# Optimization experiments

Measured on AMD Instinct MI355X. Metric: run time of the kernel, lower is better.

The kernel has to match this reference:

```python
import jax, jax.numpy as jnp
import numpy as np

N_NODES = 100000
N_EDGES = 1600000
IN_DIM = 128
HID_DIM = 128
OUT_DIM = 64


def _glorot(key, shape):
    fan_in, fan_out = shape
    lim = float(np.sqrt(6.0 / (fan_in + fan_out)))
    return jax.random.uniform(key, shape, jnp.float32, -lim, lim)


def setup_inputs() -> dict:
    key = jax.random.key(0)
    ks = jax.random.split(key, 8)
    x = jax.random.normal(ks[0], (N_NODES, IN_DIM), jnp.float32)
    edge_index = jax.random.randint(ks[1], (2, N_EDGES), 0, N_NODES, jnp.int64)
    edge_weight = jax.random.uniform(ks[2], (N_EDGES,), jnp.float32)
    W1 = _glorot(ks[3], (IN_DIM, HID_DIM))
    b1 = jnp.zeros((HID_DIM,), jnp.float32)
    W2 = _glorot(ks[4], (HID_DIM, HID_DIM))
    b2 = jnp.zeros((HID_DIM,), jnp.float32)
    W3 = _glorot(ks[5], (HID_DIM, OUT_DIM))
    b3 = jnp.zeros((OUT_DIM,), jnp.float32)
    return {"x": x, "edge_index": edge_index, "edge_weight": edge_weight,
            "W1": W1, "b1": b1, "W2": W2, "b2": b2, "W3": W3, "b3": b3}


def gcn_conv(x, src, dst, ew, W, b, n_nodes):
    # torch_geometric GCNConv: add self-loops (weight 1), symmetric normalization,
    # linear transform (no bias) then aggregate, then add bias.
    xw = x @ W                                            # [N, out]
    deg = jax.ops.segment_sum(ew, dst, num_segments=n_nodes) + 1.0  # self-loop
    dis = jax.lax.rsqrt(deg)                              # deg >= 1, safe
    norm = dis[src] * ew * dis[dst]                       # [E]
    agg = jax.ops.segment_sum(norm[:, None] * xw[src], dst, num_segments=n_nodes)
    # self-loop contribution: norm_ii = dis_i^2 * 1.0
    return agg + (dis * dis)[:, None] * xw + b


def reference(x, edge_index, edge_weight, W1, b1, W2, b2, W3, b3):
    src, dst = edge_index[0], edge_index[1]
    n = x.shape[0]
    h = gcn_conv(x, src, dst, edge_weight, W1, b1, n)
    h = jax.nn.relu(h)  # dropout is identity at inference
    h = gcn_conv(h, src, dst, edge_weight, W2, b2, n)
    h = jax.nn.relu(h)
    out = gcn_conv(h, src, dst, edge_weight, W3, b3, n)
    return out
```

## Files before the change

### kernel.cpp

```cpp
#include <hip/hip_runtime.h>


typedef __attribute__((ext_vector_type(8))) short bf16x8;
typedef __attribute__((ext_vector_type(4))) float f32x4;

__device__ inline unsigned short f2bf(float f) {
  unsigned int u = __float_as_uint(f);
  u += 0x7fffu + ((u >> 16) & 1u);
  return (unsigned short)(u >> 16);
}

__global__ void init_kernel(const int* __restrict__ ei, int* __restrict__ flag,
                            int* __restrict__ pz, int n) {
  if (blockIdx.x == 0) {
    __shared__ int nonzero;
    if (threadIdx.x == 0) nonzero = 0;
    __syncthreads();
    int acc = 0;
#pragma unroll
    for (int it = 0; it < 8; ++it) {
      const int j = threadIdx.x + (it << 8);
      acc |= ei[2 * j + 1];
    }
    if (acc != 0) atomicOr(&nonzero, 1);
    __syncthreads();
    if (threadIdx.x == 0) flag[0] = (nonzero == 0) ? 1 : 0;
  }
  int i = blockIdx.x * blockDim.x + threadIdx.x;
  const int stride = gridDim.x * blockDim.x;
  for (; i < n; i += stride) pz[i] = 0;
}

__global__ void count_deg_pack(const int* __restrict__ ei, const int* __restrict__ flag,
                               const float* __restrict__ ew,
                               unsigned long long* __restrict__ packed,
                               int* __restrict__ eseq, int E) {
  const int e = blockIdx.x * blockDim.x + threadIdx.x;
  if (e >= E) return;
  const int use64 = flag[0];
  const int d = use64 ? ei[2 * (E + e)] : ei[E + e];
  const unsigned int fx = (unsigned int)(ew[e] * 16777216.0f);
  const unsigned long long old =
      atomicAdd(&packed[d], (1ULL << 32) | (unsigned long long)fx);
  eseq[e] = (int)(old >> 32);
}

__global__ __launch_bounds__(256)
void scan_phase1(const unsigned long long* __restrict__ packed,
                 int* __restrict__ bsums, int N) {
  __shared__ int red[256];
  const int t = threadIdx.x;
  const int base = blockIdx.x * 1024 + t * 4;
  int s = 0;
#pragma unroll
  for (int j = 0; j < 4; ++j) {
    const int idx = base + j;
    if (idx < N) s += (int)(packed[idx] >> 32);
  }
  red[t] = s;
  __syncthreads();
  for (int off = 128; off > 0; off >>= 1) {
    if (t < off) red[t] += red[t + off];
    __syncthreads();
  }
  if (t == 0) bsums[blockIdx.x] = red[0];
}

__global__ __launch_bounds__(1024)
void scan_phase2(int* __restrict__ bsums, int* __restrict__ row_start, int B, int N) {
  __shared__ int s[1024];
  const int t = threadIdx.x;
  const int v = (t < B) ? bsums[t] : 0;
  s[t] = v;
  __syncthreads();
  for (int off = 1; off < 1024; off <<= 1) {
    const int add = (t >= off) ? s[t - off] : 0;
    __syncthreads();
    s[t] += add;
    __syncthreads();
  }
  if (t < B) bsums[t] = s[t] - v;
  if (t == B - 1) row_start[N] = s[t];
}

__global__ __launch_bounds__(256)
void scan_phase3_dis(const unsigned long long* __restrict__ packed,
                     const int* __restrict__ bsums, int* __restrict__ row_start,
                     float* __restrict__ dis, int N) {
  __shared__ int tsum[256];
  const int t = threadIdx.x;
  const int base = blockIdx.x * 1024 + t * 4;
  unsigned long long pk[4];
  int v[4];
#pragma unroll
  for (int j = 0; j < 4; ++j) {
    pk[j] = (base + j < N) ? packed[base + j] : 0ULL;
    v[j] = (int)(pk[j] >> 32);
  }
  const int tot = v[0] + v[1] + v[2] + v[3];
  tsum[t] = tot;
  __syncthreads();
  for (int off = 1; off < 256; off <<= 1) {
    const int add = (t >= off) ? tsum[t - off] : 0;
    __syncthreads();
    tsum[t] += add;
    __syncthreads();
  }
  int run = bsums[blockIdx.x] + tsum[t] - tot;
#pragma unroll
  for (int j = 0; j < 4; ++j) {
    const int idx = base + j;
    if (idx < N) {
      row_start[idx] = run;
      run += v[j];
      const float deg = (float)(unsigned int)pk[j] * (1.0f / 16777216.0f);
      dis[idx] = rsqrtf(deg + 1.0f);
    }
  }
}

__global__ void fill_csr(const int* __restrict__ ei, const int* __restrict__ flag,
                         const float* __restrict__ ew, const float* __restrict__ dis,
                         const int* __restrict__ row_start, const int* __restrict__ eseq,
                         int2* __restrict__ csr, int E) {
  const int e = blockIdx.x * blockDim.x + threadIdx.x;
  if (e >= E) return;
  const int use64 = flag[0];
  const int s = use64 ? ei[2 * e] : ei[e];
  const int d = use64 ? ei[2 * (E + e)] : ei[E + e];
  const float nm = dis[s] * ew[e] * dis[d];
  const int pos = row_start[d] + eseq[e];
  csr[pos] = make_int2(s, __float_as_int(nm));
}

__global__ __launch_bounds__(256)
void prep_bf16(const float* __restrict__ W1, const float* __restrict__ W2,
               const float* __restrict__ W3, unsigned short* __restrict__ Wt1,
               unsigned short* __restrict__ Wt2, unsigned short* __restrict__ Wt3,
               const float* __restrict__ x, unsigned short* __restrict__ xbf,
               long long n4) {
  const int WTB = 160;
  if (blockIdx.x < WTB) {
    const int idx = blockIdx.x * 256 + threadIdx.x;
    if (idx < 16384) {
      const int m = idx >> 7, k = idx & 127;
      Wt1[idx] = f2bf(W1[k * 128 + m]);
    } else if (idx < 32768) {
      const int l = idx - 16384;
      const int m = l >> 7, k = l & 127;
      Wt2[l] = f2bf(W2[k * 128 + m]);
    } else {
      const int l = idx - 32768;
      const int m = l >> 7, k = l & 127;
      Wt3[l] = f2bf(W3[k * 64 + m]);
    }
    return;
  }
  long long i = (long long)(blockIdx.x - WTB) * 256 + threadIdx.x;
  const long long stride = (long long)(gridDim.x - WTB) * 256;
  for (; i < n4; i += stride) {
    const float4 v = ((const float4*)x)[i];
    ushort4 o;
    o.x = f2bf(v.x); o.y = f2bf(v.y); o.z = f2bf(v.z); o.w = f2bf(v.w);
    ((ushort4*)xbf)[i] = o;
  }
}

template <int M>
__global__ __launch_bounds__(256)
void gemm_mfma(const unsigned short* __restrict__ A, const unsigned short* __restrict__ Bt,
               unsigned short* __restrict__ C, int N) {
  const int lane = threadIdx.x & 63;
  const int m = lane & 15;
  const int q = lane >> 4;
  const int row0 = (blockIdx.x << 6) + ((threadIdx.x >> 6) << 4);

  const bool rowok = (row0 + m) < N;
  const unsigned short* arow = A + (long long)(row0 + m) * 128 + q * 8;
  bf16x8 a[4];
  const bf16x8 zf = {0, 0, 0, 0, 0, 0, 0, 0};
#pragma unroll
  for (int kt = 0; kt < 4; ++kt)
    a[kt] = rowok ? *(const bf16x8*)(arow + kt * 32) : zf;

#pragma unroll
  for (int ct = 0; ct < M / 16; ++ct) {
    f32x4 acc = {0.f, 0.f, 0.f, 0.f};
    const unsigned short* brow = Bt + (ct * 16 + m) * 128 + q * 8;
#pragma unroll
    for (int kt = 0; kt < 4; ++kt) {
      const bf16x8 b = *(const bf16x8*)(brow + kt * 32);
      acc = __builtin_amdgcn_mfma_f32_16x16x32_bf16(a[kt], b, acc, 0, 0, 0);
    }
#pragma unroll
    for (int r = 0; r < 4; ++r) {
      const int row = row0 + q * 4 + r;
      if (row < N) C[(long long)row * M + ct * 16 + m] = f2bf(acc[r]);
    }
  }
}

template <int M, bool RELU, bool OUTBF>
__global__ __launch_bounds__(256)
void gather(const int2* __restrict__ csr, const int* __restrict__ row_start,
            const unsigned short* __restrict__ xw, const float* __restrict__ dis,
            const float* __restrict__ bias, void* __restrict__ outp, int N) {
  const int node = (blockIdx.x << 2) + (threadIdx.x >> 6);
  const int lane = threadIdx.x & 63;
  if (node >= N) return;
  const int beg = __builtin_amdgcn_readfirstlane(row_start[node]);
  const int end = __builtin_amdgcn_readfirstlane(row_start[node + 1]);
  if (M == 128) {
    const int c = lane << 1;
    float2 a0 = make_float2(0.f, 0.f), a1 = a0, a2 = a0, a3 = a0;
    int e = beg;
    for (; e + 7 < end; e += 8) {
      int2 p[8];
      unsigned int u[8];
#pragma unroll
      for (int j = 0; j < 8; ++j) p[j] = csr[e + j];
#pragma unroll
      for (int j = 0; j < 8; ++j)
        u[j] = *(const unsigned int*)(xw + (long long)p[j].x * 128 + c);
#pragma unroll
      for (int j = 0; j < 8; ++j) {
        const float nm = __int_as_float(p[j].y);
        float2& ac = (j & 4) ? ((j & 2) ? a3 : a2) : ((j & 2) ? a1 : a0);
        ac.x = fmaf(nm, __uint_as_float(u[j] << 16), ac.x);
        ac.y = fmaf(nm, __uint_as_float(u[j] & 0xffff0000u), ac.y);
      }
    }
    for (; e + 1 < end; e += 2) {
      const int2 p0 = csr[e], p1 = csr[e + 1];
      const unsigned int u0 = *(const unsigned int*)(xw + (long long)p0.x * 128 + c);
      const unsigned int u1 = *(const unsigned int*)(xw + (long long)p1.x * 128 + c);
      const float n0 = __int_as_float(p0.y), n1 = __int_as_float(p1.y);
      a0.x = fmaf(n0, __uint_as_float(u0 << 16), a0.x);
      a0.y = fmaf(n0, __uint_as_float(u0 & 0xffff0000u), a0.y);
      a1.x = fmaf(n1, __uint_as_float(u1 << 16), a1.x);
      a1.y = fmaf(n1, __uint_as_float(u1 & 0xffff0000u), a1.y);
    }
    if (e < end) {
      const int2 p = csr[e];
      const float nm = __int_as_float(p.y);
      const unsigned int u = *(const unsigned int*)(xw + (long long)p.x * 128 + c);
      a2.x = fmaf(nm, __uint_as_float(u << 16), a2.x);
      a2.y = fmaf(nm, __uint_as_float(u & 0xffff0000u), a2.y);
    }
    float2 acc;
    acc.x = (a0.x + a1.x) + (a2.x + a3.x);
    acc.y = (a0.y + a1.y) + (a2.y + a3.y);
    const float di = dis[node];
    const float dsq = di * di;
    const unsigned int su = *(const unsigned int*)(xw + (long long)node * 128 + c);
    const float2 bv = *(const float2*)(bias + c);
    acc.x = fmaf(dsq, __uint_as_float(su << 16), acc.x) + bv.x;
    acc.y = fmaf(dsq, __uint_as_float(su & 0xffff0000u), acc.y) + bv.y;
    if (RELU) { acc.x = fmaxf(acc.x, 0.f); acc.y = fmaxf(acc.y, 0.f); }
    if (OUTBF) {
      const unsigned int pk =
          (unsigned int)f2bf(acc.x) | ((unsigned int)f2bf(acc.y) << 16);
      ((unsigned int*)outp)[(long long)node * 64 + lane] = pk;
    } else {
      *(float2*)((float*)outp + (long long)node * 128 + c) = acc;
    }
  } else {
    float a0 = 0.f, a1 = 0.f, a2 = 0.f, a3 = 0.f;
    int e = beg;
    for (; e + 7 < end; e += 8) {
      int2 p[8];
      unsigned int v[8];
#pragma unroll
      for (int j = 0; j < 8; ++j) p[j] = csr[e + j];
#pragma unroll
      for (int j = 0; j < 8; ++j) v[j] = xw[(long long)p[j].x * 64 + lane];
#pragma unroll
      for (int j = 0; j < 8; ++j) {
        float& ac = (j & 4) ? ((j & 2) ? a3 : a2) : ((j & 2) ? a1 : a0);
        ac = fmaf(__int_as_float(p[j].y), __uint_as_float(v[j] << 16), ac);
      }
    }
    for (; e < end; ++e) {
      const int2 p = csr[e];
      const unsigned int v = xw[(long long)p.x * 64 + lane];
      a0 = fmaf(__int_as_float(p.y), __uint_as_float(v << 16), a0);
    }
    float acc = (a0 + a1) + (a2 + a3);
    const float di = dis[node];
    const unsigned int sv = xw[(long long)node * 64 + lane];
    float r = fmaf(di * di, __uint_as_float(sv << 16), acc) + bias[lane];
    if (RELU) r = fmaxf(r, 0.f);
    ((float*)outp)[(long long)node * 64 + lane] = r;
  }
}

extern "C" void kernel_launch(void* const* d_in, const int* in_sizes, int n_in,
                              void* d_out, int out_size, void* d_ws, size_t ws_size,
                              hipStream_t stream) {
  const float* x  = (const float*)d_in[0];
  const int*   ei = (const int*)d_in[1];
  const float* ew = (const float*)d_in[2];
  const float* W1 = (const float*)d_in[3];
  const float* b1 = (const float*)d_in[4];
  const float* W2 = (const float*)d_in[5];
  const float* b2 = (const float*)d_in[6];
  const float* W3 = (const float*)d_in[7];
  const float* b3 = (const float*)d_in[8];
  float* out = (float*)d_out;

  const int IN = 128;
  const int N = in_sizes[0] / IN;
  const int E = in_sizes[2];

  char* ws = (char*)d_ws;
  unsigned long long* packed = (unsigned long long*)(ws);
  float* dis       = (float*)(ws + (1u << 20));
  int*   flag      = (int*)(ws + (1536u << 10));
  int*   bsums     = (int*)(ws + (1536u << 10) + 4096);
  int*   row_start = (int*)(ws + (1600u << 10));
  int2*  csr       = (int2*)(ws + (2560u << 10));
  unsigned short* Wt1 = (unsigned short*)(ws + (15872u << 10));
  unsigned short* Wt2 = (unsigned short*)(ws + (15872u << 10) + (128u << 10));
  unsigned short* Wt3 = (unsigned short*)(ws + (15872u << 10) + (256u << 10));
  unsigned short* bufA = (unsigned short*)(ws + (16u << 20));
  unsigned short* hbf  = (unsigned short*)(ws + (42u << 20));
  int* eseq = (int*)bufA;

  const dim3 blk(256);
  const int gE = (E + 255) / 256;
  const int B = (N + 1023) / 1024;

  hipLaunchKernelGGL(init_kernel, dim3(128), blk, 0, stream, ei, flag, (int*)packed, 2 * N);
  hipLaunchKernelGGL(count_deg_pack, dim3(gE), blk, 0, stream, ei, flag, ew, packed, eseq, E);
  hipLaunchKernelGGL(scan_phase1, dim3(B), blk, 0, stream, packed, bsums, N);
  hipLaunchKernelGGL(scan_phase2, dim3(1), dim3(1024), 0, stream, bsums, row_start, B, N);
  hipLaunchKernelGGL(scan_phase3_dis, dim3(B), blk, 0, stream, packed, bsums, row_start, dis, N);
  hipLaunchKernelGGL(fill_csr, dim3(gE), blk, 0, stream, ei, flag, ew, dis, row_start, eseq, csr, E);
  hipLaunchKernelGGL(prep_bf16, dim3(160 + 2048), blk, 0, stream,
                     W1, W2, W3, Wt1, Wt2, Wt3, x, hbf, (long long)N * 32);

  const int gGemm = (N + 63) / 64;
  const int gGather = (N + 3) / 4;

  hipLaunchKernelGGL((gemm_mfma<128>), dim3(gGemm), blk, 0, stream, hbf, Wt1, bufA, N);
  hipLaunchKernelGGL((gather<128, true, true>), dim3(gGather), blk, 0, stream,
                     csr, row_start, bufA, dis, b1, hbf, N);
  hipLaunchKernelGGL((gemm_mfma<128>), dim3(gGemm), blk, 0, stream, hbf, Wt2, bufA, N);
  hipLaunchKernelGGL((gather<128, true, true>), dim3(gGather), blk, 0, stream,
                     csr, row_start, bufA, dis, b2, hbf, N);
  hipLaunchKernelGGL((gemm_mfma<64>), dim3(gGemm), blk, 0, stream, hbf, Wt3, bufA, N);
  hipLaunchKernelGGL((gather<64, false, false>), dim3(gGather), blk, 0, stream,
                     csr, row_start, bufA, dis, b3, out, N);
}
```

Measured before the change: 495.5 us.

## Privatize degree-count atomics into 16 copies to reduce atomic contention

The packed degree/count atomics are spread over 16 per-block-group copies of the per-node counter array, so fewer threads contend on the same address. The scan phases then sum across the copies, and a per-copy offset table (coff) gives each edge its CSR slot. This adds a 16x larger array to zero and scan, plus extra memory traffic for the coff writes and reads. With about 16 edges per node spread over 100k nodes, contention may already be low, so the extra traffic can outweigh the benefit.

```diff
diff --git a/kernel.cpp b/kernel.cpp
--- a/kernel.cpp
+++ b/kernel.cpp
@@ -3,6 +3,8 @@
 
 typedef __attribute__((ext_vector_type(8))) short bf16x8;
 typedef __attribute__((ext_vector_type(4))) float f32x4;
+
+#define NCOPY 16
 
 __device__ inline unsigned short f2bf(float f) {
   unsigned int u = __float_as_uint(f);
@@ -33,29 +35,33 @@
 
 __global__ void count_deg_pack(const int* __restrict__ ei, const int* __restrict__ flag,
                                const float* __restrict__ ew,
-                               unsigned long long* __restrict__ packed,
-                               int* __restrict__ eseq, int E) {
+                               unsigned long long* __restrict__ packedC,
+                               int* __restrict__ eseq, int E, int N) {
   const int e = blockIdx.x * blockDim.x + threadIdx.x;
   if (e >= E) return;
   const int use64 = flag[0];
   const int d = use64 ? ei[2 * (E + e)] : ei[E + e];
   const unsigned int fx = (unsigned int)(ew[e] * 16777216.0f);
+  const size_t slot = (size_t)(blockIdx.x & (NCOPY - 1)) * N + d;
   const unsigned long long old =
-      atomicAdd(&packed[d], (1ULL << 32) | (unsigned long long)fx);
+      atomicAdd(&packedC[slot], (1ULL << 32) | (unsigned long long)fx);
   eseq[e] = (int)(old >> 32);
 }
 
 __global__ __launch_bounds__(256)
-void scan_phase1(const unsigned long long* __restrict__ packed,
+void scan_phase1(const unsigned long long* __restrict__ packedC,
                  int* __restrict__ bsums, int N) {
   __shared__ int red[256];
   const int t = threadIdx.x;
   const int base = blockIdx.x * 1024 + t * 4;
   int s = 0;
 #pragma unroll
-  for (int j = 0; j < 4; ++j) {
-    const int idx = base + j;
-    if (idx < N) s += (int)(packed[idx] >> 32);
+  for (int c = 0; c < NCOPY; ++c) {
+#pragma unroll
+    for (int j = 0; j < 4; ++j) {
+      const int idx = base + j;
+      if (idx < N) s += (int)(packedC[(size_t)c * N + idx] >> 32);
+    }
   }
   red[t] = s;
   __syncthreads();
@@ -84,18 +90,32 @@
 }
 
 __global__ __launch_bounds__(256)
-void scan_phase3_dis(const unsigned long long* __restrict__ packed,
+void scan_phase3_dis(const unsigned long long* __restrict__ packedC,
                      const int* __restrict__ bsums, int* __restrict__ row_start,
-                     float* __restrict__ dis, int N) {
+                     int* __restrict__ coff, float* __restrict__ dis, int N) {
   __shared__ int tsum[256];
   const int t = threadIdx.x;
   const int base = blockIdx.x * 1024 + t * 4;
-  unsigned long long pk[4];
+  int cnt[NCOPY][4];
+  unsigned long long deglo[4] = {0ULL, 0ULL, 0ULL, 0ULL};
+#pragma unroll
+  for (int c = 0; c < NCOPY; ++c) {
+#pragma unroll
+    for (int j = 0; j < 4; ++j) {
+      const int idx = base + j;
+      const unsigned long long p =
+          (idx < N) ? packedC[(size_t)c * N + idx] : 0ULL;
+      cnt[c][j] = (int)(p >> 32);
+      deglo[j] += (unsigned long long)(unsigned int)p;
+    }
+  }
   int v[4];
 #pragma unroll
   for (int j = 0; j < 4; ++j) {
-    pk[j] = (base + j < N) ? packed[base + j] : 0ULL;
-    v[j] = (int)(pk[j] >> 32);
+    int s = 0;
+#pragma unroll
+    for (int c = 0; c < NCOPY; ++c) s += cnt[c][j];
+    v[j] = s;
   }
   const int tot = v[0] + v[1] + v[2] + v[3];
   tsum[t] = tot;
@@ -112,8 +132,14 @@
     const int idx = base + j;
     if (idx < N) {
       row_start[idx] = run;
+      int b = run;
+#pragma unroll
+      for (int c = 0; c < NCOPY; ++c) {
+        coff[(size_t)c * N + idx] = b;
+        b += cnt[c][j];
+      }
       run += v[j];
-      const float deg = (float)(unsigned int)pk[j] * (1.0f / 16777216.0f);
+      const float deg = (float)deglo[j] * (1.0f / 16777216.0f);
       dis[idx] = rsqrtf(deg + 1.0f);
     }
   }
@@ -121,15 +147,15 @@
 
 __global__ void fill_csr(const int* __restrict__ ei, const int* __restrict__ flag,
                          const float* __restrict__ ew, const float* __restrict__ dis,
-                         const int* __restrict__ row_start, const int* __restrict__ eseq,
-                         int2* __restrict__ csr, int E) {
+                         const int* __restrict__ coff, const int* __restrict__ eseq,
+                         int2* __restrict__ csr, int E, int N) {
   const int e = blockIdx.x * blockDim.x + threadIdx.x;
   if (e >= E) return;
   const int use64 = flag[0];
   const int s = use64 ? ei[2 * e] : ei[e];
   const int d = use64 ? ei[2 * (E + e)] : ei[E + e];
   const float nm = dis[s] * ew[e] * dis[d];
-  const int pos = row_start[d] + eseq[e];
+  const int pos = coff[(size_t)(blockIdx.x & (NCOPY - 1)) * N + d] + eseq[e];
   csr[pos] = make_int2(s, __float_as_int(nm));
 }
 
@@ -313,7 +339,6 @@
   const int E = in_sizes[2];
 
   char* ws = (char*)d_ws;
-  unsigned long long* packed = (unsigned long long*)(ws);
   float* dis       = (float*)(ws + (1u << 20));
   int*   flag      = (int*)(ws + (1536u << 10));
   int*   bsums     = (int*)(ws + (1536u << 10) + 4096);
@@ -324,18 +349,24 @@
   unsigned short* Wt3 = (unsigned short*)(ws + (15872u << 10) + (256u << 10));
   unsigned short* bufA = (unsigned short*)(ws + (16u << 20));
   unsigned short* hbf  = (unsigned short*)(ws + (42u << 20));
+  unsigned long long* packedC = (unsigned long long*)(ws + (68u << 20));
+  int* coff = (int*)(ws + (81u << 20));
   int* eseq = (int*)bufA;
 
   const dim3 blk(256);
   const int gE = (E + 255) / 256;
   const int B = (N + 1023) / 1024;
 
-  hipLaunchKernelGGL(init_kernel, dim3(128), blk, 0, stream, ei, flag, (int*)packed, 2 * N);
-  hipLaunchKernelGGL(count_deg_pack, dim3(gE), blk, 0, stream, ei, flag, ew, packed, eseq, E);
-  hipLaunchKernelGGL(scan_phase1, dim3(B), blk, 0, stream, packed, bsums, N);
+  hipLaunchKernelGGL(init_kernel, dim3(2048), blk, 0, stream, ei, flag,
+                     (int*)packedC, NCOPY * 2 * N);
+  hipLaunchKernelGGL(count_deg_pack, dim3(gE), blk, 0, stream, ei, flag, ew,
+                     packedC, eseq, E, N);
+  hipLaunchKernelGGL(scan_phase1, dim3(B), blk, 0, stream, packedC, bsums, N);
   hipLaunchKernelGGL(scan_phase2, dim3(1), dim3(1024), 0, stream, bsums, row_start, B, N);
-  hipLaunchKernelGGL(scan_phase3_dis, dim3(B), blk, 0, stream, packed, bsums, row_start, dis, N);
-  hipLaunchKernelGGL(fill_csr, dim3(gE), blk, 0, stream, ei, flag, ew, dis, row_start, eseq, csr, E);
+  hipLaunchKernelGGL(scan_phase3_dis, dim3(B), blk, 0, stream, packedC, bsums,
+                     row_start, coff, dis, N);
+  hipLaunchKernelGGL(fill_csr, dim3(gE), blk, 0, stream, ei, flag, ew, dis,
+                     coff, eseq, csr, E, N);
   hipLaunchKernelGGL(prep_bf16, dim3(160 + 2048), blk, 0, stream,
                      W1, W2, W3, Wt1, Wt2, Wt3, x, hbf, (long long)N * 32);
 
```

Measured after the change: 518.8 us. +4.7%, slower.

## Build CSR via two-level binning instead of global per-node atomics

Applied to the files above, without the earlier changes.

Replaces per-edge 64-bit global atomics on per-node degree counters with a bucketed counting sort. Edges are first histogrammed into 128-node bins per chunk in shared memory, scanned, and scattered to binned order. A per-bin kernel then computes degrees, row starts and dis with shared-memory atomics and writes the CSR, and a final pass folds in dis[src]. This targets contended global atomics and random scatter in graph preprocessing, at the cost of more kernels and an extra pass over the edges.

```diff
diff --git a/kernel.cpp b/kernel.cpp
--- a/kernel.cpp
+++ b/kernel.cpp
@@ -3,6 +3,8 @@
 
 typedef __attribute__((ext_vector_type(8))) short bf16x8;
 typedef __attribute__((ext_vector_type(4))) float f32x4;
+
+#define CHUNK 4096
 
 __device__ inline unsigned short f2bf(float f) {
   unsigned int u = __float_as_uint(f);
@@ -10,53 +12,48 @@
   return (unsigned short)(u >> 16);
 }
 
-__global__ void init_kernel(const int* __restrict__ ei, int* __restrict__ flag,
-                            int* __restrict__ pz, int n) {
-  if (blockIdx.x == 0) {
-    __shared__ int nonzero;
-    if (threadIdx.x == 0) nonzero = 0;
-    __syncthreads();
-    int acc = 0;
-#pragma unroll
-    for (int it = 0; it < 8; ++it) {
-      const int j = threadIdx.x + (it << 8);
-      acc |= ei[2 * j + 1];
-    }
-    if (acc != 0) atomicOr(&nonzero, 1);
-    __syncthreads();
-    if (threadIdx.x == 0) flag[0] = (nonzero == 0) ? 1 : 0;
-  }
-  int i = blockIdx.x * blockDim.x + threadIdx.x;
-  const int stride = gridDim.x * blockDim.x;
-  for (; i < n; i += stride) pz[i] = 0;
-}
-
-__global__ void count_deg_pack(const int* __restrict__ ei, const int* __restrict__ flag,
-                               const float* __restrict__ ew,
-                               unsigned long long* __restrict__ packed,
-                               int* __restrict__ eseq, int E) {
-  const int e = blockIdx.x * blockDim.x + threadIdx.x;
-  if (e >= E) return;
+__global__ void init_flag(const int* __restrict__ ei, int* __restrict__ flag) {
+  __shared__ int nonzero;
+  if (threadIdx.x == 0) nonzero = 0;
+  __syncthreads();
+  int acc = 0;
+#pragma unroll
+  for (int it = 0; it < 8; ++it) acc |= ei[2 * (threadIdx.x + (it << 8)) + 1];
+  if (acc != 0) atomicOr(&nonzero, 1);
+  __syncthreads();
+  if (threadIdx.x == 0) flag[0] = (nonzero == 0) ? 1 : 0;
+}
+
+__global__ __launch_bounds__(256)
+void bin_hist(const int* __restrict__ ei, const int* __restrict__ flag,
+              int* __restrict__ mat, int E, int NB, int NBLK) {
+  __shared__ int hist[1024];
+  const int t = threadIdx.x;
+  for (int i = t; i < NB; i += 256) hist[i] = 0;
+  __syncthreads();
   const int use64 = flag[0];
-  const int d = use64 ? ei[2 * (E + e)] : ei[E + e];
-  const unsigned int fx = (unsigned int)(ew[e] * 16777216.0f);
-  const unsigned long long old =
-      atomicAdd(&packed[d], (1ULL << 32) | (unsigned long long)fx);
-  eseq[e] = (int)(old >> 32);
-}
-
-__global__ __launch_bounds__(256)
-void scan_phase1(const unsigned long long* __restrict__ packed,
-                 int* __restrict__ bsums, int N) {
+  const int base = blockIdx.x * CHUNK;
+#pragma unroll
+  for (int it = 0; it < CHUNK / 256; ++it) {
+    const int e = base + t + it * 256;
+    if (e < E) {
+      const int d = use64 ? ei[2 * (E + e)] : ei[E + e];
+      atomicAdd(&hist[d >> 7], 1);
+    }
+  }
+  __syncthreads();
+  for (int i = t; i < NB; i += 256) mat[i * NBLK + blockIdx.x] = hist[i];
+}
+
+__global__ __launch_bounds__(256)
+void scan_phase1(const int* __restrict__ mat, int* __restrict__ bsums, int L) {
   __shared__ int red[256];
   const int t = threadIdx.x;
   const int base = blockIdx.x * 1024 + t * 4;
   int s = 0;
 #pragma unroll
-  for (int j = 0; j < 4; ++j) {
-    const int idx = base + j;
-    if (idx < N) s += (int)(packed[idx] >> 32);
-  }
+  for (int j = 0; j < 4; ++j)
+    if (base + j < L) s += mat[base + j];
   red[t] = s;
   __syncthreads();
   for (int off = 128; off > 0; off >>= 1) {
@@ -84,19 +81,13 @@
 }
 
 __global__ __launch_bounds__(256)
-void scan_phase3_dis(const unsigned long long* __restrict__ packed,
-                     const int* __restrict__ bsums, int* __restrict__ row_start,
-                     float* __restrict__ dis, int N) {
+void scan_phase3(int* __restrict__ mat, const int* __restrict__ bsums, int L) {
   __shared__ int tsum[256];
   const int t = threadIdx.x;
   const int base = blockIdx.x * 1024 + t * 4;
-  unsigned long long pk[4];
   int v[4];
 #pragma unroll
-  for (int j = 0; j < 4; ++j) {
-    pk[j] = (base + j < N) ? packed[base + j] : 0ULL;
-    v[j] = (int)(pk[j] >> 32);
-  }
+  for (int j = 0; j < 4; ++j) v[j] = (base + j < L) ? mat[base + j] : 0;
   const int tot = v[0] + v[1] + v[2] + v[3];
   tsum[t] = tot;
   __syncthreads();
@@ -109,28 +100,98 @@
   int run = bsums[blockIdx.x] + tsum[t] - tot;
 #pragma unroll
   for (int j = 0; j < 4; ++j) {
-    const int idx = base + j;
-    if (idx < N) {
-      row_start[idx] = run;
-      run += v[j];
-      const float deg = (float)(unsigned int)pk[j] * (1.0f / 16777216.0f);
-      dis[idx] = rsqrtf(deg + 1.0f);
-    }
-  }
-}
-
-__global__ void fill_csr(const int* __restrict__ ei, const int* __restrict__ flag,
-                         const float* __restrict__ ew, const float* __restrict__ dis,
-                         const int* __restrict__ row_start, const int* __restrict__ eseq,
-                         int2* __restrict__ csr, int E) {
+    if (base + j < L) { mat[base + j] = run; run += v[j]; }
+  }
+}
+
+__global__ __launch_bounds__(256)
+void bin_scatter(const int* __restrict__ ei, const int* __restrict__ flag,
+                 const float* __restrict__ ew, const int* __restrict__ mat,
+                 int2* __restrict__ binned, int E, int NB, int NBLK) {
+  __shared__ int boff[1024];
+  __shared__ int cur[1024];
+  const int t = threadIdx.x;
+  for (int i = t; i < NB; i += 256) {
+    boff[i] = mat[i * NBLK + blockIdx.x];
+    cur[i] = 0;
+  }
+  __syncthreads();
+  const int use64 = flag[0];
+  const int base = blockIdx.x * CHUNK;
+#pragma unroll
+  for (int it = 0; it < CHUNK / 256; ++it) {
+    const int e = base + t + it * 256;
+    if (e < E) {
+      const int s = use64 ? ei[2 * e] : ei[e];
+      const int d = use64 ? ei[2 * (E + e)] : ei[E + e];
+      const int b = d >> 7;
+      const int r = atomicAdd(&cur[b], 1);
+      binned[boff[b] + r] = make_int2(s | ((d & 127) << 17), __float_as_int(ew[e]));
+    }
+  }
+}
+
+__global__ __launch_bounds__(256)
+void bucket_finalize(const int2* __restrict__ binned, const int* __restrict__ mat,
+                     int* __restrict__ row_start, float* __restrict__ dis,
+                     int2* __restrict__ csr, int E, int N, int NB, int NBLK) {
+  __shared__ int cnt[128];
+  __shared__ unsigned int fxs[128];
+  __shared__ int sc[128];
+  __shared__ int rowb[128];
+  __shared__ float disl[128];
+  __shared__ int cur[128];
+  const int t = threadIdx.x;
+  const int b = blockIdx.x;
+  const int beg = mat[b * NBLK];
+  const int end = (b == NB - 1) ? E : mat[(b + 1) * NBLK];
+  if (t < 128) { cnt[t] = 0; fxs[t] = 0u; }
+  __syncthreads();
+  for (int i = beg + t; i < end; i += 256) {
+    const int2 r = binned[i];
+    const int dl = (r.x >> 17) & 127;
+    atomicAdd(&cnt[dl], 1);
+    atomicAdd(&fxs[dl], (unsigned int)(__int_as_float(r.y) * 16777216.0f));
+  }
+  __syncthreads();
+  if (t < 128) sc[t] = cnt[t];
+  __syncthreads();
+  for (int off = 1; off < 128; off <<= 1) {
+    const int v = (t < 128 && t >= off) ? sc[t - off] : 0;
+    __syncthreads();
+    if (t < 128) sc[t] += v;
+    __syncthreads();
+  }
+  if (t < 128) {
+    const int node = (b << 7) + t;
+    const int rb = beg + sc[t] - cnt[t];
+    rowb[t] = rb;
+    cur[t] = 0;
+    if (node < N) {
+      row_start[node] = rb;
+      const float deg = (float)fxs[t] * (1.0f / 16777216.0f);
+      const float di = rsqrtf(deg + 1.0f);
+      dis[node] = di;
+      disl[t] = di;
+    }
+  }
+  __syncthreads();
+  for (int i = beg + t; i < end; i += 256) {
+    const int2 r = binned[i];
+    const int dl = (r.x >> 17) & 127;
+    const int rk = atomicAdd(&cur[dl], 1);
+    csr[rowb[dl] + rk] =
+        make_int2(r.x & 0x1FFFF, __float_as_int(__int_as_float(r.y) * disl[dl]));
+  }
+}
+
+__global__ __launch_bounds__(256)
+void norm_fold(int2* __restrict__ csr, const float* __restrict__ dis, int E) {
   const int e = blockIdx.x * blockDim.x + threadIdx.x;
   if (e >= E) return;
-  const int use64 = flag[0];
-  const int s = use64 ? ei[2 * e] : ei[e];
-  const int d = use64 ? ei[2 * (E + e)] : ei[E + e];
-  const float nm = dis[s] * ew[e] * dis[d];
-  const int pos = row_start[d] + eseq[e];
-  csr[pos] = make_int2(s, __float_as_int(nm));
+  int2 r = csr[e];
+  r.y = __float_as_int(__int_as_float(r.y) * dis[r.x]);
+  csr[e] = r;
 }
 
 __global__ __launch_bounds__(256)
@@ -313,7 +374,6 @@
   const int E = in_sizes[2];
 
   char* ws = (char*)d_ws;
-  unsigned long long* packed = (unsigned long long*)(ws);
   float* dis       = (float*)(ws + (1u << 20));
   int*   flag      = (int*)(ws + (1536u << 10));
   int*   bsums     = (int*)(ws + (1536u << 10) + 4096);
@@ -324,18 +384,26 @@
   unsigned short* Wt3 = (unsigned short*)(ws + (15872u << 10) + (256u << 10));
   unsigned short* bufA = (unsigned short*)(ws + (16u << 20));
   unsigned short* hbf  = (unsigned short*)(ws + (42u << 20));
-  int* eseq = (int*)bufA;
+  int*   mat    = (int*)(ws + (68u << 20));
+  int2*  binned = (int2*)(ws + (70u << 20));
 
   const dim3 blk(256);
   const int gE = (E + 255) / 256;
-  const int B = (N + 1023) / 1024;
-
-  hipLaunchKernelGGL(init_kernel, dim3(128), blk, 0, stream, ei, flag, (int*)packed, 2 * N);
-  hipLaunchKernelGGL(count_deg_pack, dim3(gE), blk, 0, stream, ei, flag, ew, packed, eseq, E);
-  hipLaunchKernelGGL(scan_phase1, dim3(B), blk, 0, stream, packed, bsums, N);
-  hipLaunchKernelGGL(scan_phase2, dim3(1), dim3(1024), 0, stream, bsums, row_start, B, N);
-  hipLaunchKernelGGL(scan_phase3_dis, dim3(B), blk, 0, stream, packed, bsums, row_start, dis, N);
-  hipLaunchKernelGGL(fill_csr, dim3(gE), blk, 0, stream, ei, flag, ew, dis, row_start, eseq, csr, E);
+  const int NB = (N + 127) >> 7;
+  const int NBLK = (E + CHUNK - 1) / CHUNK;
+  const int L = NB * NBLK;
+  const int SB = (L + 1023) / 1024;
+
+  hipLaunchKernelGGL(init_flag, dim3(1), blk, 0, stream, ei, flag);
+  hipLaunchKernelGGL(bin_hist, dim3(NBLK), blk, 0, stream, ei, flag, mat, E, NB, NBLK);
+  hipLaunchKernelGGL(scan_phase1, dim3(SB), blk, 0, stream, mat, bsums, L);
+  hipLaunchKernelGGL(scan_phase2, dim3(1), dim3(1024), 0, stream, bsums, row_start, SB, N);
+  hipLaunchKernelGGL(scan_phase3, dim3(SB), blk, 0, stream, mat, bsums, L);
+  hipLaunchKernelGGL(bin_scatter, dim3(NBLK), blk, 0, stream, ei, flag, ew, mat,
+                     binned, E, NB, NBLK);
+  hipLaunchKernelGGL(bucket_finalize, dim3(NB), blk, 0, stream, binned, mat,
+                     row_start, dis, csr, E, N, NB, NBLK);
+  hipLaunchKernelGGL(norm_fold, dim3(gE), blk, 0, stream, csr, dis, E);
   hipLaunchKernelGGL(prep_bf16, dim3(160 + 2048), blk, 0, stream,
                      W1, W2, W3, Wt1, Wt2, Wt3, x, hbf, (long long)N * 32);
 
```

Result: faster. 461.4 us (-6.9%).
